# Optimization experiments

Measured on AMD Instinct MI355X. Metric: run time of the kernel, lower is better.

Reference implementation:

```python
import jax, jax.numpy as jnp
import numpy as np

N = 20000          # nodes
E = 320000         # edges (avg degree 16)
F_IN = 512         # in_channels
HID = 64           # hidden_channels
H1 = 8             # conv1 heads (hard-coded in source)
C_OUT = 7          # out_channels (num classes)
OUT2 = C_OUT * C_OUT  # conv2 per-head output dim = out_channels**2
H2 = 8             # conv2 heads
NC = 64            # number of clusters
NIDX = 10000       # |cluster_index|
NEG_SLOPE = 0.2    # PyG GATConv default leaky-relu slope


def gat_conv(x, edge_index, W, att_src, att_dst, bias, concat):
    """PyG GATConv (add_self_loops=True, eval mode so attention dropout is off)."""
    n = x.shape[0]
    H, C = att_src.shape
    h = (x @ W).reshape(n, H, C)                      # [n, H, C]
    loop = jnp.arange(n)
    src = jnp.concatenate([edge_index[0], loop])      # self loops appended
    dst = jnp.concatenate([edge_index[1], loop])
    a_src = jnp.einsum('nhc,hc->nh', h, att_src)      # [n, H]
    a_dst = jnp.einsum('nhc,hc->nh', h, att_dst)
    e = jax.nn.leaky_relu(a_src[src] + a_dst[dst], NEG_SLOPE)   # [Etot, H]
    # segment softmax over incoming edges of each destination node
    m = jax.lax.stop_gradient(jax.ops.segment_max(e, dst, num_segments=n))
    p = jnp.exp(e - m[dst])
    denom = jax.ops.segment_sum(p, dst, num_segments=n)
    alpha = p / denom[dst]                            # [Etot, H]
    out = jax.ops.segment_sum(alpha[:, :, None] * h[src], dst, num_segments=n)  # [n, H, C]
    if concat:
        return out.reshape(n, H * C) + bias
    return out.mean(axis=1) + bias


def setup_inputs() -> dict:
    key = jax.random.key(0)
    ks = jax.random.split(key, 12)
    s1 = 1.0 / np.sqrt(F_IN)
    s2 = 1.0 / np.sqrt(2 * HID * H1)
    return {
        'x': jax.random.normal(ks[0], (N, F_IN), dtype=jnp.float32),
        'edge_index': jax.random.randint(ks[1], (2, E), 0, N),
        'cluster_id': jax.random.uniform(ks[2], (N, NC), dtype=jnp.float32),
        'cluster_index': jax.random.randint(ks[3], (NIDX,), 0, N),
        'W1': jax.random.normal(ks[4], (F_IN, H1 * HID), dtype=jnp.float32) * s1,
        'att_src1': jax.random.normal(ks[5], (H1, HID), dtype=jnp.float32) * 0.1,
        'att_dst1': jax.random.normal(ks[6], (H1, HID), dtype=jnp.float32) * 0.1,
        'b1': jnp.zeros((H1 * HID,), dtype=jnp.float32),
        'W2': jax.random.normal(ks[7], (2 * H1 * HID, H2 * OUT2), dtype=jnp.float32) * s2,
        'att_src2': jax.random.normal(ks[8], (H2, OUT2), dtype=jnp.float32) * 0.1,
        'att_dst2': jax.random.normal(ks[9], (H2, OUT2), dtype=jnp.float32) * 0.1,
        'b2': jnp.zeros((OUT2,), dtype=jnp.float32),
    }


def reference(x, edge_index, cluster_id, cluster_index,
              W1, att_src1, att_dst1, b1, W2, att_src2, att_dst2, b2):
    n = x.shape[0]
    # eval mode: F.dropout and attention dropout are identity
    h = jax.nn.elu(gat_conv(x, edge_index, W1, att_src1, att_dst1, b1, concat=True))  # [N, H1*HID]
    cid = cluster_id[cluster_index]                       # [NIDX, NC]
    cluster_features = (cid.T @ h[cluster_index]) / cid.sum(0)[:, None]  # [NC, H1*HID]
    x1 = cluster_features[jnp.argmax(cluster_id, axis=1)] # [N, H1*HID]
    xx = jnp.concatenate([jnp.concatenate([h, x1], 1),
                          jnp.concatenate([x1, h], 1)], 0)  # [2N, 2*H1*HID]
    ei2 = jnp.concatenate([edge_index, edge_index + n], 1)  # doubled graph
    return gat_conv(xx, ei2, W2, att_src2, att_dst2, b2, concat=False)  # [2N, OUT2]
```

## Files before the change

kernel.cpp:

```cpp
#include <hip/hip_runtime.h>

#define NNODES 20000
#define MPAD   20096
#define NEDGES 320000
#define FIN    512
#define HC1    512
#define NHEAD  8
#define OUT2   49
#define NCOL2  392
#define NB2    784
#define NPAD2  896
#define NCLU   64
#define NIDX   10000
#define NEG    0.2f

typedef unsigned short u16;
typedef short bf16x8 __attribute__((ext_vector_type(8)));
typedef float f32x4 __attribute__((ext_vector_type(4)));

static __device__ __forceinline__ float lrelu(float v){ return v > 0.f ? v : NEG*v; }

static __device__ __forceinline__ u16 f2bf_hi(float f, float& rem) {
  union { float f; unsigned u; } c; c.f = f;
  unsigned hb = c.u & 0xFFFF0000u;
  union { unsigned u; float f; } d; d.u = hb;
  rem = f - d.f;
  return (u16)(hb >> 16);
}
static __device__ __forceinline__ u16 f2bf(float f) {
  union { float f; unsigned u; } c; c.f = f;
  return (u16)(c.u >> 16);
}
static __device__ __forceinline__ u16 f2bf_rn(float f) {
  union { float f; unsigned u; } c; c.f = f;
  unsigned r = c.u + 0x7FFFu + ((c.u >> 16) & 1u);
  return (u16)(r >> 16);
}
static __device__ __forceinline__ float bf2f(u16 u) {
  union { unsigned u; float f; } c; c.u = ((unsigned)u) << 16;
  return c.f;
}
static __device__ __forceinline__ void load8bf(const u16* p, float* o) {
  ushort4 a = *(const ushort4*)p;
  ushort4 b = *(const ushort4*)(p + 4);
  o[0]=bf2f(a.x); o[1]=bf2f(a.y); o[2]=bf2f(a.z); o[3]=bf2f(a.w);
  o[4]=bf2f(b.x); o[5]=bf2f(b.y); o[6]=bf2f(b.z); o[7]=bf2f(b.w);
}

typedef __attribute__((address_space(3))) unsigned int lds_u32;
typedef __attribute__((address_space(1))) const unsigned int glb_u32;
static __device__ __forceinline__ void gl_lds16(const u16* g, u16* l) {
  __builtin_amdgcn_global_load_lds((glb_u32*)g, (lds_u32*)l, 16, 0, 0);
}

__global__ __launch_bounds__(256) void split4_kernel(const float* __restrict__ x,
                                                     u16* __restrict__ xh, u16* __restrict__ xl) {
  __shared__ __align__(16) u16 th[4][512], tl[4][512];
  int wv = threadIdx.x >> 6;
  int lane = threadIdx.x & 63;
  int i = blockIdx.x*4 + wv;
  const float* p = x + (size_t)i*FIN + lane*8;
  float4 v0 = *(const float4*)p, v1 = *(const float4*)(p+4);
  float rem; ushort4 h0,h1,l0,l1;
  h0.x = f2bf_hi(v0.x, rem); l0.x = f2bf(rem);
  h0.y = f2bf_hi(v0.y, rem); l0.y = f2bf(rem);
  h0.z = f2bf_hi(v0.z, rem); l0.z = f2bf(rem);
  h0.w = f2bf_hi(v0.w, rem); l0.w = f2bf(rem);
  h1.x = f2bf_hi(v1.x, rem); l1.x = f2bf(rem);
  h1.y = f2bf_hi(v1.y, rem); l1.y = f2bf(rem);
  h1.z = f2bf_hi(v1.z, rem); l1.z = f2bf(rem);
  h1.w = f2bf_hi(v1.w, rem); l1.w = f2bf(rem);
  *(ushort4*)&th[wv][lane*8]   = h0; *(ushort4*)&th[wv][lane*8+4] = h1;
  *(ushort4*)&tl[wv][lane*8]   = l0; *(ushort4*)&tl[wv][lane*8+4] = l1;
  __syncthreads();
  int kc = threadIdx.x >> 2, nd = threadIdx.x & 3;
  size_t o = ((size_t)kc*MPAD + blockIdx.x*4 + nd)*8;
  *(uint4*)&xh[o] = *(const uint4*)&th[nd][kc*8];
  *(uint4*)&xl[o] = *(const uint4*)&tl[nd][kc*8];
}

__global__ void tw1_kernel(const float* __restrict__ W1, u16* __restrict__ Th, u16* __restrict__ Tl) {
  int tid = blockIdx.x*256 + threadIdx.x;
  int kc = tid >> 9, j = tid & 511;
  float rem; ushort4 h0,h1,l0,l1;
  h0.x = f2bf_hi(W1[(size_t)(kc*8+0)*512 + j], rem); l0.x = f2bf(rem);
  h0.y = f2bf_hi(W1[(size_t)(kc*8+1)*512 + j], rem); l0.y = f2bf(rem);
  h0.z = f2bf_hi(W1[(size_t)(kc*8+2)*512 + j], rem); l0.z = f2bf(rem);
  h0.w = f2bf_hi(W1[(size_t)(kc*8+3)*512 + j], rem); l0.w = f2bf(rem);
  h1.x = f2bf_hi(W1[(size_t)(kc*8+4)*512 + j], rem); l1.x = f2bf(rem);
  h1.y = f2bf_hi(W1[(size_t)(kc*8+5)*512 + j], rem); l1.y = f2bf(rem);
  h1.z = f2bf_hi(W1[(size_t)(kc*8+6)*512 + j], rem); l1.z = f2bf(rem);
  h1.w = f2bf_hi(W1[(size_t)(kc*8+7)*512 + j], rem); l1.w = f2bf(rem);
  size_t o = ((size_t)kc*512 + j)*8;
  *(ushort4*)&Th[o] = h0; *(ushort4*)&Th[o+4] = h1;
  *(ushort4*)&Tl[o] = l0; *(ushort4*)&Tl[o+4] = l1;
}

__global__ void tb2_kernel(const float* __restrict__ W2, u16* __restrict__ Th, u16* __restrict__ Tl) {
  int tid = blockIdx.x*256 + threadIdx.x;
  int kc = tid / NPAD2, j = tid - kc*NPAD2;
  float v[8];
  #pragma unroll
  for (int e = 0; e < 8; e++) {
    int k = kc*8 + e;
    v[e] = (j < NCOL2) ? W2[(size_t)k*NCOL2 + j]
         : ((j < NB2) ? W2[(size_t)(512+k)*NCOL2 + (j - NCOL2)] : 0.f);
  }
  float rem; ushort4 h0,h1,l0,l1;
  h0.x = f2bf_hi(v[0], rem); l0.x = f2bf(rem);
  h0.y = f2bf_hi(v[1], rem); l0.y = f2bf(rem);
  h0.z = f2bf_hi(v[2], rem); l0.z = f2bf(rem);
  h0.w = f2bf_hi(v[3], rem); l0.w = f2bf(rem);
  h1.x = f2bf_hi(v[4], rem); l1.x = f2bf(rem);
  h1.y = f2bf_hi(v[5], rem); l1.y = f2bf(rem);
  h1.z = f2bf_hi(v[6], rem); l1.z = f2bf(rem);
  h1.w = f2bf_hi(v[7], rem); l1.w = f2bf(rem);
  size_t o = ((size_t)kc*NPAD2 + j)*8;
  *(ushort4*)&Th[o] = h0; *(ushort4*)&Th[o+4] = h1;
  *(ushort4*)&Tl[o] = l0; *(ushort4*)&Tl[o+4] = l1;
}

template<int EPI>
__global__ __launch_bounds__(256) void gemm_mfma(
    const u16* __restrict__ Ah, const u16* __restrict__ Al,
    const u16* __restrict__ Bh, const u16* __restrict__ Bl,
    int Apitch, int Bpitch,
    u16* __restrict__ Cbf, int M, int Ncols,
    const int* __restrict__ cmax, const float* __restrict__ CFW, u16* __restrict__ h2)
{
  __shared__ __align__(16) u16 S[16512];
  int tid = threadIdx.x;
  int lane = tid & 63;
  int w = tid >> 6;
  int row0 = blockIdx.x * 128;
  int col0 = blockIdx.y * 128;

  const u16* G; size_t pitch; int lb;
  if      (w == 0) { G = Ah + ((size_t)row0 + lane)*8; pitch = (size_t)Apitch; lb = 0; }
  else if (w == 1) { G = Al + ((size_t)row0 + lane)*8; pitch = (size_t)Apitch; lb = 4128; }
  else if (w == 2) { G = Bh + ((size_t)col0 + lane)*8; pitch = (size_t)Bpitch; lb = 8256; }
  else             { G = Bl + ((size_t)col0 + lane)*8; pitch = (size_t)Bpitch; lb = 12384; }

  int wr = (w >> 1) * 64;
  int wc = (w & 1) * 64;
  int l16 = lane & 15;
  int q = lane >> 4;

  f32x4 acc[4][4];
  #pragma unroll
  for (int i = 0; i < 4; i++)
    #pragma unroll
    for (int j = 0; j < 4; j++)
      acc[i][j] = (f32x4){0.f, 0.f, 0.f, 0.f};

  for (int t = 0; t < 16; t++) {
    #pragma unroll
    for (int c = 0; c < 4; c++) {
      const u16* g = G + ((size_t)(t*4 + c))*pitch*8;
      gl_lds16(g,       &S[lb + c*1032]);
      gl_lds16(g + 512, &S[lb + c*1032 + 512]);
    }
    __syncthreads();
    bf16x8 ah[4], al[4], bh[4], bl[4];
    #pragma unroll
    for (int i = 0; i < 4; i++) {
      int ra = q*1032 + (wr + i*16 + l16)*8;
      int rb = q*1032 + (wc + i*16 + l16)*8;
      ah[i] = *(const bf16x8*)&S[ra];
      al[i] = *(const bf16x8*)&S[4128 + ra];
      bh[i] = *(const bf16x8*)&S[8256 + rb];
      bl[i] = *(const bf16x8*)&S[12384 + rb];
    }
    #pragma unroll
    for (int i = 0; i < 4; i++)
      #pragma unroll
      for (int j = 0; j < 4; j++)
        acc[i][j] = __builtin_amdgcn_mfma_f32_16x16x32_bf16(ah[i], bh[j], acc[i][j], 0, 0, 0);
    #pragma unroll
    for (int i = 0; i < 4; i++)
      #pragma unroll
      for (int j = 0; j < 4; j++)
        acc[i][j] = __builtin_amdgcn_mfma_f32_16x16x32_bf16(ah[i], bl[j], acc[i][j], 0, 0, 0);
    #pragma unroll
    for (int i = 0; i < 4; i++)
      #pragma unroll
      for (int j = 0; j < 4; j++)
        acc[i][j] = __builtin_amdgcn_mfma_f32_16x16x32_bf16(al[i], bh[j], acc[i][j], 0, 0, 0);
    __syncthreads();
  }

  if (EPI == 0) {
    #pragma unroll
    for (int i = 0; i < 4; i++) {
      #pragma unroll
      for (int r = 0; r < 4; r++) {
        int m = row0 + wr + i*16 + q*4 + r;
        if (m < M) {
          #pragma unroll
          for (int j = 0; j < 4; j++)
            Cbf[(size_t)m*Ncols + col0 + wc + j*16 + l16] = f2bf_rn(acc[i][j][r]);
        }
      }
    }
  } else {
    #pragma unroll
    for (int i = 0; i < 4; i++) {
      #pragma unroll
      for (int r = 0; r < 4; r++) {
        int m = row0 + wr + i*16 + q*4 + r;
        if (m >= M) continue;
        int c = cmax[m];
        const float* cf = CFW + (size_t)c * NB2;
        #pragma unroll
        for (int j = 0; j < 4; j++) {
          int n = col0 + wc + j*16 + l16;
          if (n >= NB2) continue;
          float v = acc[i][j][r];
          if (n < NCOL2) h2[(size_t)m*NCOL2 + n] = f2bf_rn(v + cf[NCOL2 + n]);
          else           h2[(size_t)(NNODES + m)*NCOL2 + (n - NCOL2)] = f2bf_rn(v + cf[n - NCOL2]);
        }
      }
    }
  }
}

__global__ void hist_kernel(const int* __restrict__ ei, int* __restrict__ counts) {
  int e = blockIdx.x*256 + threadIdx.x;
  if (e < NEDGES) atomicAdd(&counts[ei[NEDGES + e]], 1);
}

__global__ __launch_bounds__(1024) void scan_kernel(const int* __restrict__ counts,
                                                    int* __restrict__ rowptr, int* __restrict__ cursor) {
  __shared__ int part[1024];
  int t = threadIdx.x;
  const int CH = 20;
  int start = t*CH;
  int end = min(start+CH, NNODES);
  int sum = 0;
  for (int i = start; i < end; i++) sum += counts[i];
  part[t] = sum;
  __syncthreads();
  for (int off = 1; off < 1024; off <<= 1) {
    int v = part[t];
    int add = (t >= off) ? part[t-off] : 0;
    __syncthreads();
    part[t] = v + add;
    __syncthreads();
  }
  int run = part[t] - sum;
  for (int i = start; i < end; i++) {
    rowptr[i] = run; cursor[i] = run;
    run += counts[i];
  }
  if (t == 1023) rowptr[NNODES] = part[1023];
}

__global__ void scatter_kernel(const int* __restrict__ ei, int* __restrict__ cursor,
                               int* __restrict__ csr, int* __restrict__ dstid) {
  int e = blockIdx.x*256 + threadIdx.x;
  if (e < NEDGES) {
    int src = ei[e];
    int dst = ei[NEDGES + e];
    int pos = atomicAdd(&cursor[dst], 1);
    csr[pos] = src;
    dstid[pos] = dst;
  }
}

__global__ __launch_bounds__(256) void a1_kernel(
    const u16* __restrict__ hpre, const float* __restrict__ atts, const float* __restrict__ attd,
    float* __restrict__ as1, float* __restrict__ ad1)
{
  int lane = threadIdx.x & 63;
  int i = blockIdx.x*4 + (threadIdx.x >> 6);
  float hv[8];
  load8bf(hpre + (size_t)i*HC1 + lane*8, hv);
  const float* ap = atts + lane*8; const float* dp = attd + lane*8;
  float ps = 0.f, pd = 0.f;
  #pragma unroll
  for (int k = 0; k < 8; k++) { ps = fmaf(hv[k], ap[k], ps); pd = fmaf(hv[k], dp[k], pd); }
  ps += __shfl_down(ps, 4, 8); ps += __shfl_down(ps, 2, 8); ps += __shfl_down(ps, 1, 8);
  pd += __shfl_down(pd, 4, 8); pd += __shfl_down(pd, 2, 8); pd += __shfl_down(pd, 1, 8);
  if ((lane & 7) == 0) {
    as1[i*8 + (lane >> 3)] = ps;
    ad1[i*8 + (lane >> 3)] = pd;
  }
}

__global__ void exp1_kernel(const int* __restrict__ csr, const int* __restrict__ dstid,
                            const float* __restrict__ as1, const float* __restrict__ ad1,
                            float* __restrict__ p1)
{
  int pos = blockIdx.x*256 + threadIdx.x;
  int src = csr[pos], dst = dstid[pos];
  const float* a = as1 + (size_t)src*8;
  const float* d = ad1 + (size_t)dst*8;
  float4 a0 = *(const float4*)a, a1v = *(const float4*)(a+4);
  float4 d0 = *(const float4*)d, d1v = *(const float4*)(d+4);
  float4 o0, o1;
  o0.x = __expf(lrelu(a0.x + d0.x));  o0.y = __expf(lrelu(a0.y + d0.y));
  o0.z = __expf(lrelu(a0.z + d0.z));  o0.w = __expf(lrelu(a0.w + d0.w));
  o1.x = __expf(lrelu(a1v.x + d1v.x)); o1.y = __expf(lrelu(a1v.y + d1v.y));
  o1.z = __expf(lrelu(a1v.z + d1v.z)); o1.w = __expf(lrelu(a1v.w + d1v.w));
  *(float4*)(p1 + (size_t)pos*8)     = o0;
  *(float4*)(p1 + (size_t)pos*8 + 4) = o1;
}

__global__ void exp2_kernel(const int* __restrict__ csr, const int* __restrict__ dstid,
                            const float* __restrict__ as2, const float* __restrict__ ad2,
                            float* __restrict__ p2)
{
  int pos2 = blockIdx.x*256 + threadIdx.x;
  int half = (pos2 >= NEDGES) ? 1 : 0;
  int pos = pos2 - half*NEDGES;
  int src = csr[pos] + half*NNODES;
  int dst = dstid[pos] + half*NNODES;
  const float* a = as2 + (size_t)src*8;
  const float* d = ad2 + (size_t)dst*8;
  float4 a0 = *(const float4*)a, a1v = *(const float4*)(a+4);
  float4 d0 = *(const float4*)d, d1v = *(const float4*)(d+4);
  float4 o0, o1;
  o0.x = __expf(lrelu(a0.x + d0.x));  o0.y = __expf(lrelu(a0.y + d0.y));
  o0.z = __expf(lrelu(a0.z + d0.z));  o0.w = __expf(lrelu(a0.w + d0.w));
  o1.x = __expf(lrelu(a1v.x + d1v.x)); o1.y = __expf(lrelu(a1v.y + d1v.y));
  o1.z = __expf(lrelu(a1v.z + d1v.z)); o1.w = __expf(lrelu(a1v.w + d1v.w));
  *(float4*)(p2 + (size_t)pos2*8)     = o0;
  *(float4*)(p2 + (size_t)pos2*8 + 4) = o1;
}

__global__ __launch_bounds__(256) void agg1_kernel(
    const u16* __restrict__ hpre, const float* __restrict__ p1,
    const float* __restrict__ as1, const float* __restrict__ ad1,
    const int* __restrict__ rowptr, const int* __restrict__ csr, const float* __restrict__ b1,
    u16* __restrict__ hhr, u16* __restrict__ hlr,
    u16* __restrict__ hh, u16* __restrict__ hl)
{
  __shared__ __align__(16) u16 sh[4][512], sl[4][512];
  int lane = threadIdx.x & 63;
  int wv = threadIdx.x >> 6;
  int i = blockIdx.x*4 + wv;
  int hd = lane >> 3;
  int rs = rowptr[i];
  int deg = rowptr[i+1] - rs;
  float selfp = __expf(lrelu(as1[i*8 + hd] + ad1[i*8 + hd]));
  float acc[8];
  {
    float v[8];
    load8bf(hpre + (size_t)i*HC1 + lane*8, v);
    #pragma unroll
    for (int k = 0; k < 8; k++) acc[k] = selfp * v[k];
  }
  float s = selfp;
  int j = 0;
  for (; j + 1 < deg; j += 2) {
    int s0 = csr[rs+j], s1 = csr[rs+j+1];
    float w0 = p1[(size_t)(rs+j)*8 + hd];
    float w1 = p1[(size_t)(rs+j+1)*8 + hd];
    float v0[8], v1[8];
    load8bf(hpre + (size_t)s0*HC1 + lane*8, v0);
    load8bf(hpre + (size_t)s1*HC1 + lane*8, v1);
    #pragma unroll
    for (int k = 0; k < 8; k++) acc[k] = fmaf(w0, v0[k], acc[k]);
    #pragma unroll
    for (int k = 0; k < 8; k++) acc[k] = fmaf(w1, v1[k], acc[k]);
    s += w0 + w1;
  }
  if (j < deg) {
    int s0 = csr[rs+j];
    float w0 = p1[(size_t)(rs+j)*8 + hd];
    float v0[8];
    load8bf(hpre + (size_t)s0*HC1 + lane*8, v0);
    #pragma unroll
    for (int k = 0; k < 8; k++) acc[k] = fmaf(w0, v0[k], acc[k]);
    s += w0;
  }
  float inv = 1.f / s;
  float rem; ushort4 h0,h1,l0,l1;
  float o[8];
  #pragma unroll
  for (int k = 0; k < 8; k++) {
    float v = acc[k]*inv + b1[lane*8 + k];
    o[k] = v > 0.f ? v : __expf(v) - 1.f;
  }
  h0.x = f2bf_hi(o[0], rem); l0.x = f2bf(rem);
  h0.y = f2bf_hi(o[1], rem); l0.y = f2bf(rem);
  h0.z = f2bf_hi(o[2], rem); l0.z = f2bf(rem);
  h0.w = f2bf_hi(o[3], rem); l0.w = f2bf(rem);
  h1.x = f2bf_hi(o[4], rem); l1.x = f2bf(rem);
  h1.y = f2bf_hi(o[5], rem); l1.y = f2bf(rem);
  h1.z = f2bf_hi(o[6], rem); l1.z = f2bf(rem);
  h1.w = f2bf_hi(o[7], rem); l1.w = f2bf(rem);
  size_t rb = (size_t)i*HC1 + lane*8;
  *(ushort4*)&hhr[rb]   = h0; *(ushort4*)&hhr[rb+4] = h1;
  *(ushort4*)&hlr[rb]   = l0; *(ushort4*)&hlr[rb+4] = l1;
  *(ushort4*)&sh[wv][lane*8]   = h0; *(ushort4*)&sh[wv][lane*8+4] = h1;
  *(ushort4*)&sl[wv][lane*8]   = l0; *(ushort4*)&sl[wv][lane*8+4] = l1;
  __syncthreads();
  int kc = threadIdx.x >> 2, nd = threadIdx.x & 3;
  size_t po = ((size_t)kc*MPAD + blockIdx.x*4 + nd)*8;
  *(uint4*)&hh[po] = *(const uint4*)&sh[nd][kc*8];
  *(uint4*)&hl[po] = *(const uint4*)&sl[nd][kc*8];
}

__global__ __launch_bounds__(256) void colsum_kernel(
    const float* __restrict__ cluster_id, const int* __restrict__ cidx, float* __restrict__ colsum)
{
  __shared__ float part[4][64];
  int tid = threadIdx.x; int q = tid >> 6, col = tid & 63;
  int start = blockIdx.x*313, end = min(start+313, NIDX);
  float acc = 0.f;
  for (int t = start + q; t < end; t += 4) {
    int node = cidx[t];
    acc += cluster_id[(size_t)node*NCLU + col];
  }
  part[q][col] = acc;
  __syncthreads();
  if (tid < 64) {
    float v = part[0][tid] + part[1][tid] + part[2][tid] + part[3][tid];
    atomicAdd(&colsum[tid], v);
  }
}

__global__ __launch_bounds__(256) void cf_kernel(
    const float* __restrict__ cluster_id, const int* __restrict__ cidx,
    const u16* __restrict__ hhr, const u16* __restrict__ hlr, float* __restrict__ CFraw)
{
  int chl = threadIdx.x & 63;
  int cq  = threadIdx.x >> 6;
  int chg = blockIdx.x*64 + chl;
  int start = blockIdx.y*400, end = start + 400;
  float acc[16];
  #pragma unroll
  for (int k = 0; k < 16; k++) acc[k] = 0.f;
  #pragma unroll 2
  for (int t = start; t < end; t++) {
    int node = cidx[t];
    size_t hi = (size_t)node*HC1 + chg;
    float hv = bf2f(hhr[hi]) + bf2f(hlr[hi]);
    const float* cp = cluster_id + (size_t)node*NCLU + cq*16;
    float4 c0 = *(const float4*)cp,     c1 = *(const float4*)(cp+4);
    float4 c2 = *(const float4*)(cp+8), c3 = *(const float4*)(cp+12);
    acc[0]  = fmaf(c0.x, hv, acc[0]);  acc[1]  = fmaf(c0.y, hv, acc[1]);
    acc[2]  = fmaf(c0.z, hv, acc[2]);  acc[3]  = fmaf(c0.w, hv, acc[3]);
    acc[4]  = fmaf(c1.x, hv, acc[4]);  acc[5]  = fmaf(c1.y, hv, acc[5]);
    acc[6]  = fmaf(c1.z, hv, acc[6]);  acc[7]  = fmaf(c1.w, hv, acc[7]);
    acc[8]  = fmaf(c2.x, hv, acc[8]);  acc[9]  = fmaf(c2.y, hv, acc[9]);
    acc[10] = fmaf(c2.z, hv, acc[10]); acc[11] = fmaf(c2.w, hv, acc[11]);
    acc[12] = fmaf(c3.x, hv, acc[12]); acc[13] = fmaf(c3.y, hv, acc[13]);
    acc[14] = fmaf(c3.z, hv, acc[14]); acc[15] = fmaf(c3.w, hv, acc[15]);
  }
  #pragma unroll
  for (int k = 0; k < 16; k++)
    atomicAdd(&CFraw[(size_t)(cq*16 + k)*HC1 + chg], acc[k]);
}

__global__ __launch_bounds__(256) void argmax_kernel(const float* __restrict__ cluster_id, int* __restrict__ cmax)
{
  int lane = threadIdx.x & 63;
  int i = blockIdx.x*4 + (threadIdx.x >> 6);
  float v = cluster_id[(size_t)i*NCLU + lane];
  int idx = lane;
  #pragma unroll
  for (int off = 32; off > 0; off >>= 1) {
    float ov = __shfl_xor(v, off);
    int oi = __shfl_xor(idx, off);
    if (ov > v || (ov == v && oi < idx)) { v = ov; idx = oi; }
  }
  if (lane == 0) cmax[i] = idx;
}

__global__ __launch_bounds__(256) void cfw_kernel(
    const float* __restrict__ CFraw, const float* __restrict__ colsum,
    const float* __restrict__ W2, float* __restrict__ CFW)
{
  int o = blockIdx.x*256 + threadIdx.x;
  int c = o / NB2, j = o - c*NB2;
  const float* src = (j < NCOL2) ? (W2 + j) : (W2 + (size_t)512*NCOL2 + (j - NCOL2));
  float acc = 0.f;
  for (int k = 0; k < 512; k++) acc = fmaf(CFraw[(size_t)c*512 + k], src[(size_t)k*NCOL2], acc);
  CFW[o] = acc / colsum[c];
}

__global__ __launch_bounds__(256) void a2_kernel(
    const u16* __restrict__ h2, const float* __restrict__ atts, const float* __restrict__ attd,
    float* __restrict__ as2, float* __restrict__ ad2)
{
  __shared__ float rows[32*NCOL2];
  __shared__ float sa[NCOL2], sd[NCOL2];
  int tid = threadIdx.x;
  size_t base = (size_t)blockIdx.x * 32 * NCOL2;
  for (int idx = tid; idx < 32*NCOL2; idx += 256) rows[idx] = bf2f(h2[base + idx]);
  for (int idx = tid; idx < NCOL2; idx += 256) { sa[idx] = atts[idx]; sd[idx] = attd[idx]; }
  __syncthreads();
  int r = tid >> 3, hd = tid & 7;
  const float* rp = rows + r*NCOL2 + hd*OUT2;
  const float* ap = sa + hd*OUT2;
  const float* dp = sd + hd*OUT2;
  float ps = 0.f, pd = 0.f;
  #pragma unroll
  for (int j = 0; j < OUT2; j++) { float v = rp[j]; ps = fmaf(v, ap[j], ps); pd = fmaf(v, dp[j], pd); }
  int node = blockIdx.x*32 + r;
  as2[node*8 + hd] = ps;
  ad2[node*8 + hd] = pd;
}

__global__ __launch_bounds__(256) void agg2_kernel(
    const u16* __restrict__ h2, const float* __restrict__ p2,
    const float* __restrict__ as2, const float* __restrict__ ad2,
    const int* __restrict__ rowptr, const int* __restrict__ csr, const float* __restrict__ b2,
    float* __restrict__ out)
{
  __shared__ float red[4][NCOL2];
  int lane = threadIdx.x & 63;
  int w = threadIdx.x >> 6;
  int u = blockIdx.x*4 + w;
  int bn = (u < NNODES) ? u : u - NNODES;
  int off = u - bn;
  int rs = rowptr[bn];
  int deg = rowptr[bn+1] - rs;
  size_t pbase = (size_t)rs + (off ? NEDGES : 0);
  int hd = lane >> 3, sub = lane & 7;
  int cbase = hd*OUT2 + sub;
  float selfp = __expf(lrelu(as2[u*8 + hd] + ad2[u*8 + hd]));
  float acc[7];
  {
    const u16* own = h2 + (size_t)u*NCOL2 + cbase;
    #pragma unroll
    for (int k = 0; k < 7; k++)
      acc[k] = (sub + 8*k < OUT2) ? selfp * bf2f(own[8*k]) : 0.f;
  }
  float s = selfp;
  int j = 0;
  for (; j + 3 < deg; j += 4) {
    int s0 = csr[rs+j]   + off, s1 = csr[rs+j+1] + off;
    int s2 = csr[rs+j+2] + off, s3 = csr[rs+j+3] + off;
    float w0 = p2[(pbase+j)*8   + hd], w1 = p2[(pbase+j+1)*8 + hd];
    float w2 = p2[(pbase+j+2)*8 + hd], w3 = p2[(pbase+j+3)*8 + hd];
    const u16* r0 = h2 + (size_t)s0*NCOL2 + cbase;
    const u16* r1 = h2 + (size_t)s1*NCOL2 + cbase;
    const u16* r2 = h2 + (size_t)s2*NCOL2 + cbase;
    const u16* r3 = h2 + (size_t)s3*NCOL2 + cbase;
    #pragma unroll
    for (int k = 0; k < 7; k++) {
      if (sub + 8*k < OUT2) {
        acc[k] = fmaf(w0, bf2f(r0[8*k]), acc[k]);
        acc[k] = fmaf(w1, bf2f(r1[8*k]), acc[k]);
        acc[k] = fmaf(w2, bf2f(r2[8*k]), acc[k]);
        acc[k] = fmaf(w3, bf2f(r3[8*k]), acc[k]);
      }
    }
    s += (w0 + w1) + (w2 + w3);
  }
  for (; j < deg; j++) {
    int s0 = csr[rs+j] + off;
    float w0 = p2[(pbase+j)*8 + hd];
    const u16* r0 = h2 + (size_t)s0*NCOL2 + cbase;
    #pragma unroll
    for (int k = 0; k < 7; k++)
      if (sub + 8*k < OUT2) acc[k] = fmaf(w0, bf2f(r0[8*k]), acc[k]);
    s += w0;
  }
  float inv = 1.f / s;
  #pragma unroll
  for (int k = 0; k < 7; k++)
    if (sub + 8*k < OUT2) red[w][cbase + 8*k] = acc[k] * inv;
  __syncthreads();
  if (lane < OUT2) {
    float t = 0.f;
    #pragma unroll
    for (int h = 0; h < 8; h++) t += red[w][h*OUT2 + lane];
    out[(size_t)u*OUT2 + lane] = 0.125f*t + b2[lane];
  }
}

extern "C" void kernel_launch(void* const* d_in, const int* in_sizes, int n_in,
                              void* d_out, int out_size, void* d_ws, size_t ws_size,
                              hipStream_t stream)
{
  (void)in_sizes; (void)n_in; (void)out_size; (void)ws_size;
  const float* x     = (const float*)d_in[0];
  const int*   ei    = (const int*)d_in[1];
  const float* cid   = (const float*)d_in[2];
  const int*   cidx  = (const int*)d_in[3];
  const float* W1    = (const float*)d_in[4];
  const float* atts1 = (const float*)d_in[5];
  const float* attd1 = (const float*)d_in[6];
  const float* b1    = (const float*)d_in[7];
  const float* W2    = (const float*)d_in[8];
  const float* atts2 = (const float*)d_in[9];
  const float* attd2 = (const float*)d_in[10];
  const float* b2    = (const float*)d_in[11];
  float* out = (float*)d_out;

  char* ws = (char*)d_ws;
  size_t off = 0;
  auto alloc = [&](size_t b){ size_t r = off; off += (b + 255) & ~(size_t)255; return r; };
  size_t o_hpre = alloc((size_t)NNODES*HC1*2);
  size_t o_h2   = alloc((size_t)2*NNODES*NCOL2*2);
  size_t o_xh   = alloc((size_t)64*MPAD*8*2);
  size_t o_xl   = alloc((size_t)64*MPAD*8*2);
  size_t o_hh   = alloc((size_t)64*MPAD*8*2);
  size_t o_hl   = alloc((size_t)64*MPAD*8*2);
  size_t o_hhr  = alloc((size_t)NNODES*HC1*2);
  size_t o_hlr  = alloc((size_t)NNODES*HC1*2);
  size_t o_w1h  = alloc((size_t)64*512*8*2);
  size_t o_w1l  = alloc((size_t)64*512*8*2);
  size_t o_b2h  = alloc((size_t)64*NPAD2*8*2);
  size_t o_b2l  = alloc((size_t)64*NPAD2*8*2);
  size_t o_CFW  = alloc((size_t)NCLU*NB2*4);
  size_t o_as1  = alloc((size_t)NNODES*8*4);
  size_t o_ad1  = alloc((size_t)NNODES*8*4);
  size_t o_as2  = alloc((size_t)2*NNODES*8*4);
  size_t o_ad2  = alloc((size_t)2*NNODES*8*4);
  size_t o_p1   = alloc((size_t)NEDGES*8*4);
  size_t o_p2   = alloc((size_t)2*NEDGES*8*4);
  size_t o_rp   = alloc((size_t)(NNODES+1)*4);
  size_t o_cur  = alloc((size_t)NNODES*4);
  size_t o_csr  = alloc((size_t)NEDGES*4);
  size_t o_dst  = alloc((size_t)NEDGES*4);
  size_t o_cmax = alloc((size_t)NNODES*4);
  size_t o_cnt  = alloc((size_t)NNODES*4);
  size_t o_csum = alloc(256 + (size_t)NCLU*HC1*4);

  u16*   hpre  = (u16*)(ws + o_hpre);
  u16*   h2    = (u16*)(ws + o_h2);
  u16*   xh    = (u16*)(ws + o_xh);
  u16*   xl    = (u16*)(ws + o_xl);
  u16*   hh    = (u16*)(ws + o_hh);
  u16*   hl    = (u16*)(ws + o_hl);
  u16*   hhr   = (u16*)(ws + o_hhr);
  u16*   hlr   = (u16*)(ws + o_hlr);
  u16*   w1h   = (u16*)(ws + o_w1h);
  u16*   w1l   = (u16*)(ws + o_w1l);
  u16*   b2h   = (u16*)(ws + o_b2h);
  u16*   b2l   = (u16*)(ws + o_b2l);
  float* CFW   = (float*)(ws + o_CFW);
  float* as1   = (float*)(ws + o_as1);
  float* ad1   = (float*)(ws + o_ad1);
  float* as2   = (float*)(ws + o_as2);
  float* ad2   = (float*)(ws + o_ad2);
  float* p1    = (float*)(ws + o_p1);
  float* p2    = (float*)(ws + o_p2);
  int*   rp    = (int*)(ws + o_rp);
  int*   cur   = (int*)(ws + o_cur);
  int*   csr   = (int*)(ws + o_csr);
  int*   dstid = (int*)(ws + o_dst);
  int*   cmax  = (int*)(ws + o_cmax);
  int*   cnt   = (int*)(ws + o_cnt);
  float* colsum= (float*)(ws + o_csum);
  float* CFraw = (float*)(ws + o_csum + 256);

  hipMemsetAsync(ws + o_cnt, 0, (size_t)NNODES*4, stream);
  hipMemsetAsync(ws + o_csum, 0, 256 + (size_t)NCLU*HC1*4, stream);

  split4_kernel<<<5000, 256, 0, stream>>>(x, xh, xl);
  tw1_kernel<<<128, 256, 0, stream>>>(W1, w1h, w1l);
  tb2_kernel<<<224, 256, 0, stream>>>(W2, b2h, b2l);
  hist_kernel<<<1250, 256, 0, stream>>>(ei, cnt);
  scan_kernel<<<1, 1024, 0, stream>>>(cnt, rp, cur);
  scatter_kernel<<<1250, 256, 0, stream>>>(ei, cur, csr, dstid);
  gemm_mfma<0><<<dim3(157,4), 256, 0, stream>>>(xh, xl, w1h, w1l, MPAD, 512, hpre, NNODES, 512, nullptr, nullptr, nullptr);
  a1_kernel<<<5000, 256, 0, stream>>>(hpre, atts1, attd1, as1, ad1);
  exp1_kernel<<<1250, 256, 0, stream>>>(csr, dstid, as1, ad1, p1);
  agg1_kernel<<<5000, 256, 0, stream>>>(hpre, p1, as1, ad1, rp, csr, b1, hhr, hlr, hh, hl);
  colsum_kernel<<<32, 256, 0, stream>>>(cid, cidx, colsum);
  cf_kernel<<<dim3(8,25), 256, 0, stream>>>(cid, cidx, hhr, hlr, CFraw);
  argmax_kernel<<<5000, 256, 0, stream>>>(cid, cmax);
  cfw_kernel<<<196, 256, 0, stream>>>(CFraw, colsum, W2, CFW);
  gemm_mfma<1><<<dim3(157,7), 256, 0, stream>>>(hh, hl, b2h, b2l, MPAD, NPAD2, nullptr, NNODES, NB2, cmax, CFW, h2);
  a2_kernel<<<1250, 256, 0, stream>>>(h2, atts2, attd2, as2, ad2);
  exp2_kernel<<<2500, 256, 0, stream>>>(csr, dstid, as2, ad2, p2);
  agg2_kernel<<<10000, 256, 0, stream>>>(h2, p2, as2, ad2, rp, csr, b2, out);
}
```

Before: 689.9 us.

## Double-buffer LDS tiles in MFMA GEMM to overlap global loads with compute

The bf16 split-precision GEMM now uses two LDS buffers. The next k-tile's global-to-LDS loads are issued right after the barrier, before the MFMAs on the current tile run, and the trailing barrier is dropped. The intent is to hide global load latency behind matrix compute. In exchange, the 1032-element row padding is removed and LDS per block roughly doubles, which may lower occupancy.

```diff
diff --git a/kernel.cpp b/kernel.cpp
--- a/kernel.cpp
+++ b/kernel.cpp
@@ -128,18 +128,19 @@
     u16* __restrict__ Cbf, int M, int Ncols,
     const int* __restrict__ cmax, const float* __restrict__ CFW, u16* __restrict__ h2)
 {
-  __shared__ __align__(16) u16 S[16512];
+  __shared__ __align__(16) u16 S[2][16384];
   int tid = threadIdx.x;
   int lane = tid & 63;
   int w = tid >> 6;
   int row0 = blockIdx.x * 128;
   int col0 = blockIdx.y * 128;
 
-  const u16* G; size_t pitch; int lb;
-  if      (w == 0) { G = Ah + ((size_t)row0 + lane)*8; pitch = (size_t)Apitch; lb = 0; }
-  else if (w == 1) { G = Al + ((size_t)row0 + lane)*8; pitch = (size_t)Apitch; lb = 4128; }
-  else if (w == 2) { G = Bh + ((size_t)col0 + lane)*8; pitch = (size_t)Bpitch; lb = 8256; }
-  else             { G = Bl + ((size_t)col0 + lane)*8; pitch = (size_t)Bpitch; lb = 12384; }
+  const u16* G; size_t pitch;
+  if      (w == 0) { G = Ah + ((size_t)row0 + lane)*8; pitch = (size_t)Apitch; }
+  else if (w == 1) { G = Al + ((size_t)row0 + lane)*8; pitch = (size_t)Apitch; }
+  else if (w == 2) { G = Bh + ((size_t)col0 + lane)*8; pitch = (size_t)Bpitch; }
+  else             { G = Bl + ((size_t)col0 + lane)*8; pitch = (size_t)Bpitch; }
+  int lb = w * 4096;
 
   int wr = (w >> 1) * 64;
   int wc = (w & 1) * 64;
@@ -153,23 +154,34 @@
     for (int j = 0; j < 4; j++)
       acc[i][j] = (f32x4){0.f, 0.f, 0.f, 0.f};
 
+  #pragma unroll
+  for (int c = 0; c < 4; c++) {
+    const u16* g = G + ((size_t)c)*pitch*8;
+    gl_lds16(g,       &S[0][lb + c*1024]);
+    gl_lds16(g + 512, &S[0][lb + c*1024 + 512]);
+  }
+
   for (int t = 0; t < 16; t++) {
-    #pragma unroll
-    for (int c = 0; c < 4; c++) {
-      const u16* g = G + ((size_t)(t*4 + c))*pitch*8;
-      gl_lds16(g,       &S[lb + c*1032]);
-      gl_lds16(g + 512, &S[lb + c*1032 + 512]);
+    int cur = t & 1;
+    __syncthreads();
+    if (t < 15) {
+      #pragma unroll
+      for (int c = 0; c < 4; c++) {
+        const u16* g = G + ((size_t)((t+1)*4 + c))*pitch*8;
+        gl_lds16(g,       &S[1-cur][lb + c*1024]);
+        gl_lds16(g + 512, &S[1-cur][lb + c*1024 + 512]);
+      }
     }
-    __syncthreads();
+    const u16* P = S[cur];
     bf16x8 ah[4], al[4], bh[4], bl[4];
     #pragma unroll
     for (int i = 0; i < 4; i++) {
-      int ra = q*1032 + (wr + i*16 + l16)*8;
-      int rb = q*1032 + (wc + i*16 + l16)*8;
-      ah[i] = *(const bf16x8*)&S[ra];
-      al[i] = *(const bf16x8*)&S[4128 + ra];
-      bh[i] = *(const bf16x8*)&S[8256 + rb];
-      bl[i] = *(const bf16x8*)&S[12384 + rb];
+      int ra = q*1024 + (wr + i*16 + l16)*8;
+      int rb = q*1024 + (wc + i*16 + l16)*8;
+      ah[i] = *(const bf16x8*)&P[ra];
+      al[i] = *(const bf16x8*)&P[4096 + ra];
+      bh[i] = *(const bf16x8*)&P[8192 + rb];
+      bl[i] = *(const bf16x8*)&P[12288 + rb];
     }
     #pragma unroll
     for (int i = 0; i < 4; i++)
@@ -186,7 +198,6 @@
       #pragma unroll
       for (int j = 0; j < 4; j++)
         acc[i][j] = __builtin_amdgcn_mfma_f32_16x16x32_bf16(al[i], bh[j], acc[i][j], 0, 0, 0);
-    __syncthreads();
   }
 
   if (EPI == 0) {
```

New measurement: 692.9 us. About the same (+0.4%).
